# Kernel optimization log

Hardware: AMD Instinct MI355X
Metric: run time of the kernel (lower is better)

Reference implementation:

```python
import jax, jax.numpy as jnp
import numpy as np

# ---- architecture constants ----
SENSOR = 128          # u feature width
B_LAYERS = 5          # branch MLP: 4 tanh hidden + 1 linear out
B_UNITS = 1024
LORA = 64
TU = 128              # trunk hidden units
TL = 4                # trunk dense layers
TRUNK_DIMS = [1] + [TU] * (TL - 1) + [1]   # 1 -> 128 -> 128 -> 128 -> 1
NO_TRUNK_PARAMS = sum(d_out + d_in * d_out for d_in, d_out in zip(TRUNK_DIMS[:-1], TRUNK_DIMS[1:]))  # 33409
T0, TFINAL = 0.0, 1.0
BATCH = 2048


def setup_inputs() -> dict:
    key = jax.random.key(0)
    ks = jax.random.split(key, 16)
    def glorot(k, shape):
        fan_in, fan_out = shape[0], shape[1]
        s = jnp.sqrt(2.0 / (fan_in + fan_out)).astype(jnp.float32)
        return jax.random.normal(k, shape, dtype=jnp.float32) * s
    inp = {
        "t": jax.random.uniform(ks[0], (BATCH, 1), dtype=jnp.float32),
        "u": jax.random.normal(ks[1], (BATCH, SENSOR), dtype=jnp.float32),
        # branch MLP: Dense(1024)+tanh x4, then Dense(1024)
        "bw0": glorot(ks[2], (SENSOR, B_UNITS)), "bb0": jnp.zeros((B_UNITS,), jnp.float32),
        "bw1": glorot(ks[3], (B_UNITS, B_UNITS)), "bb1": jnp.zeros((B_UNITS,), jnp.float32),
        "bw2": glorot(ks[4], (B_UNITS, B_UNITS)), "bb2": jnp.zeros((B_UNITS,), jnp.float32),
        "bw3": glorot(ks[5], (B_UNITS, B_UNITS)), "bb3": jnp.zeros((B_UNITS,), jnp.float32),
        "bw4": glorot(ks[6], (B_UNITS, B_UNITS)), "bb4": jnp.zeros((B_UNITS,), jnp.float32),
        # LoRA factors generating trunk params
        "W1": glorot(ks[7], (B_UNITS, LORA)),
        "W2": glorot(ks[8], (LORA, NO_TRUNK_PARAMS)),
    }
    return inp


def _slice_trunk(p):
    """Split per-sample flat trunk params [B,P] into (kernel,bias) per layer.
    Flax tree_flatten order per Dense: bias then kernel."""
    layers = []
    k = 0
    for d_in, d_out in zip(TRUNK_DIMS[:-1], TRUNK_DIMS[1:]):
        b = p[:, k:k + d_out]; k += d_out
        W = p[:, k:k + d_in * d_out].reshape(-1, d_in, d_out); k += d_in * d_out
        layers.append((W, b))
    return layers


def reference(t, u, bw0, bb0, bw1, bb1, bw2, bb2, bw3, bb3, bw4, bb4, W1, W2):
    q0 = u[:, :1]                                     # [B,1]
    # branch MLP (hypernetwork body)
    net = u
    for W, b in ((bw0, bb0), (bw1, bb1), (bw2, bb2), (bw3, bb3)):
        net = jnp.tanh(net @ W + b)
    net = net @ bw4 + bb4                             # [B, units]
    # LoRA-generated per-sample trunk params
    params = net @ (W1 @ W2)                          # [B, NO_TRUNK_PARAMS]
    # batched per-sample trunk MLP on t[i] (vectorized form of the Python loop)
    x = t                                             # [B,1]
    trunk_layers = _slice_trunk(params)
    for i, (W, b) in enumerate(trunk_layers):
        x = jnp.einsum('bi,bio->bo', x, W) + b
        if i < TL - 1:
            x = jnp.tanh(x)
    q = x                                             # [B,1]
    # hard constraint: u0 + (t-t0)/(tfinal-t0)*nn
    out = q0 + (t - T0) / (TFINAL - T0) * q           # [B,1]
    return out.reshape(-1)
```

## Files before the change

kernel.cpp:

```cpp
#include <hip/hip_runtime.h>
#include <hip/hip_bf16.h>
#include <stdint.h>

typedef unsigned short u16;
typedef unsigned int   u32;
typedef short s16x8 __attribute__((ext_vector_type(8)));
typedef float f32x4 __attribute__((ext_vector_type(4)));

#define LDP 33409

__device__ __forceinline__ u16 f2bf(float f) {
    union { float f; u32 u; } v; v.f = f;
    u32 r = v.u + 0x7fffu + ((v.u >> 16) & 1u);
    return (u16)(r >> 16);
}
__device__ __forceinline__ float bf2f(u16 h) {
    union { u32 u; float f; } v; v.u = ((u32)h) << 16;
    return v.f;
}
__device__ __forceinline__ float fast_tanh(float x) {
    float e = __expf(2.0f * x);
    return 1.0f - 2.0f / (e + 1.0f);
}
__device__ __forceinline__ f32x4 MFMA(s16x8 a, s16x8 b, f32x4 c) {
    return __builtin_amdgcn_mfma_f32_16x16x32_bf16(a, b, c, 0, 0, 0);
}
__device__ __forceinline__ void gload_lds16(const void* g, void* l) {
    __builtin_amdgcn_global_load_lds(
        (const __attribute__((address_space(1))) u32*)(uintptr_t)g,
        (__attribute__((address_space(3))) u32*)(uintptr_t)l, 16, 0, 0);
}

__global__ __launch_bounds__(256, 2)
void gemm_l0(const float* __restrict__ u, const float* __restrict__ bw0,
             const float* __restrict__ bias, u16* __restrict__ Cout,
             const float* __restrict__ bw1, u16* __restrict__ bw1t)
{
    __shared__ __align__(16) char lds[24576];
    const int bid = blockIdx.x, tid = threadIdx.x;

    if (bid < 256) {
        u16 (*As)[128 * 32] = (u16(*)[128 * 32])lds;
        u16 (*Bs)[64 * 32]  = (u16(*)[64 * 32])(lds + 16384);
        const int lane = tid & 63, wid = tid >> 6;
        const int wr = wid >> 1, wc = wid & 1;
        const int bn = (bid & 15) * 64, bm = (bid >> 4) * 128;
        f32x4 acc[4][2] = {};

        auto STAGE = [&](int buf, int t) {
            const int k0 = t << 5;
            #pragma unroll
            for (int r = 0; r < 2; ++r) {
                int idx = r * 256 + tid;
                int row = idx >> 2, ck = idx & 3;
                const float* src = u + (size_t)(bm + row) * 128 + k0 + ck * 8;
                float4 x = *(const float4*)src;
                float4 y = *(const float4*)(src + 4);
                u16 o8[8] = {f2bf(x.x), f2bf(x.y), f2bf(x.z), f2bf(x.w),
                             f2bf(y.x), f2bf(y.y), f2bf(y.z), f2bf(y.w)};
                *(s16x8*)&As[buf][row * 32 + ((ck ^ (row & 3)) << 3)] = *(s16x8*)o8;
            }
            {
                int kk = tid >> 3, cg = tid & 7;
                const float* src = bw0 + (size_t)(k0 + kk) * 1024 + bn + cg * 8;
                float4 x = *(const float4*)src;
                float4 y = *(const float4*)(src + 4);
                float v[8] = {x.x, x.y, x.z, x.w, y.x, y.y, y.z, y.w};
                const int c = kk >> 3, e = kk & 7;
                #pragma unroll
                for (int j = 0; j < 8; ++j) {
                    int col = cg * 8 + j;
                    Bs[buf][col * 32 + ((c ^ (col & 3)) << 3) + e] = f2bf(v[j]);
                }
            }
        };
        auto COMPUTE = [&](int buf) {
            s16x8 av[4], bv[2];
            #pragma unroll
            for (int mi = 0; mi < 4; ++mi) {
                int row = wr * 64 + mi * 16 + (lane & 15);
                int s = (lane >> 4) ^ (row & 3);
                av[mi] = *(const s16x8*)&As[buf][row * 32 + s * 8];
            }
            #pragma unroll
            for (int ni = 0; ni < 2; ++ni) {
                int col = wc * 32 + ni * 16 + (lane & 15);
                int s = (lane >> 4) ^ (col & 3);
                bv[ni] = *(const s16x8*)&Bs[buf][col * 32 + s * 8];
            }
            #pragma unroll
            for (int mi = 0; mi < 4; ++mi)
            #pragma unroll
            for (int ni = 0; ni < 2; ++ni)
                acc[mi][ni] = MFMA(av[mi], bv[ni], acc[mi][ni]);
        };

        STAGE(0, 0);
        __syncthreads();
        #pragma unroll
        for (int t = 0; t < 4; ++t) {
            if (t + 1 < 4) STAGE((t + 1) & 1, t + 1);
            COMPUTE(t & 1);
            __syncthreads();
        }
        #pragma unroll
        for (int mi = 0; mi < 4; ++mi)
        #pragma unroll
        for (int ni = 0; ni < 2; ++ni) {
            const int col = bn + wc * 32 + ni * 16 + (lane & 15);
            const float bv = bias[col];
            #pragma unroll
            for (int jj = 0; jj < 4; ++jj) {
                const int row = bm + wr * 64 + mi * 16 + (lane >> 4) * 4 + jj;
                Cout[(size_t)row * 1024 + col] = f2bf(fast_tanh(acc[mi][ni][jj] + bv));
            }
        }
    } else {
        float (*tile)[65] = (float(*)[65])lds;
        const int idx = bid - 256;
        const int rb = (idx >> 4) * 64, cb = (idx & 15) * 64;
        for (int i = tid; i < 64 * 64; i += 256) {
            int r = i >> 6, c = i & 63;
            tile[r][c] = bw1[(size_t)(rb + r) * 1024 + cb + c];
        }
        __syncthreads();
        for (int i = tid; i < 64 * 64; i += 256) {
            int c = i >> 6, r = i & 63;
            bw1t[(size_t)(cb + c) * 1024 + rb + r] = f2bf(tile[r][c]);
        }
    }
}

__global__ __launch_bounds__(256, 2)
void gemm_fused(const u16* __restrict__ A, int lda,
                const u16* __restrict__ Bt, int ldb,
                const float* __restrict__ bias,
                u16* __restrict__ Cout, int ldc, int K, int mode,
                const float* __restrict__ xsrc, u16* __restrict__ xdst,
                const float* __restrict__ bw4, const float* __restrict__ bb4,
                const float* __restrict__ W1, u16* __restrict__ BWt,
                float* __restrict__ bz,
                const float* __restrict__ W2, u16* __restrict__ Btb)
{
    __shared__ __align__(16) char lds[24576];
    const int bid = blockIdx.x, tid = threadIdx.x;

    if (bid < 256) {
        u16 (*As)[128 * 32] = (u16(*)[128 * 32])lds;
        u16 (*Bs)[64 * 32]  = (u16(*)[64 * 32])(lds + 16384);
        const int lane = tid & 63, wid = tid >> 6;
        const int wr = wid >> 1, wc = wid & 1;
        const int bn = (bid & 15) * 64, bm = (bid >> 4) * 128;
        const int NT = K >> 5;
        const int arow = tid >> 2, ck = tid & 3;
        const u16* aSrc = A + (size_t)(bm + arow) * lda + (ck ^ (arow & 3)) * 8;
        const u16* bSrc = Bt + (size_t)(bn + arow) * ldb + (ck ^ (arow & 3)) * 8;
        const size_t aHalf = (size_t)64 * lda;
        f32x4 acc[4][2] = {};

        auto STAGE = [&](int buf, int t) {
            const int k0 = t << 5;
            gload_lds16(aSrc + k0,         (char*)As[buf] + wid * 1024);
            gload_lds16(aSrc + aHalf + k0, (char*)As[buf] + 4096 + wid * 1024);
            gload_lds16(bSrc + k0,         (char*)Bs[buf] + wid * 1024);
        };
        auto COMPUTE = [&](int buf) {
            s16x8 av[4], bv[2];
            #pragma unroll
            for (int mi = 0; mi < 4; ++mi) {
                int row = wr * 64 + mi * 16 + (lane & 15);
                int s = (lane >> 4) ^ (row & 3);
                av[mi] = *(const s16x8*)&As[buf][row * 32 + s * 8];
            }
            #pragma unroll
            for (int ni = 0; ni < 2; ++ni) {
                int col = wc * 32 + ni * 16 + (lane & 15);
                int s = (lane >> 4) ^ (col & 3);
                bv[ni] = *(const s16x8*)&Bs[buf][col * 32 + s * 8];
            }
            #pragma unroll
            for (int mi = 0; mi < 4; ++mi)
            #pragma unroll
            for (int ni = 0; ni < 2; ++ni)
                acc[mi][ni] = MFMA(av[mi], bv[ni], acc[mi][ni]);
        };

        STAGE(0, 0);
        __syncthreads();
        for (int t = 0; t < NT; ++t) {
            if (t + 1 < NT) STAGE((t + 1) & 1, t + 1);
            COMPUTE(t & 1);
            __syncthreads();
        }
        #pragma unroll
        for (int mi = 0; mi < 4; ++mi)
        #pragma unroll
        for (int ni = 0; ni < 2; ++ni) {
            const int col = bn + wc * 32 + ni * 16 + (lane & 15);
            const float bv = bias[col];
            #pragma unroll
            for (int jj = 0; jj < 4; ++jj) {
                const int row = bm + wr * 64 + mi * 16 + (lane >> 4) * 4 + jj;
                Cout[(size_t)row * ldc + col] = f2bf(fast_tanh(acc[mi][ni][jj] + bv));
            }
        }
    } else if (mode <= 2 && bid < 512) {
        float (*tile)[65] = (float(*)[65])lds;
        const int idx = bid - 256;
        const int rb = (idx >> 4) * 64, cb = (idx & 15) * 64;
        for (int i = tid; i < 64 * 64; i += 256) {
            int r = i >> 6, c = i & 63;
            tile[r][c] = xsrc[(size_t)(rb + r) * 1024 + cb + c];
        }
        __syncthreads();
        for (int i = tid; i < 64 * 64; i += 256) {
            int c = i >> 6, r = i & 63;
            xdst[(size_t)(cb + c) * 1024 + rb + r] = f2bf(tile[r][c]);
        }
    } else if (mode == 2) {
        const int lb = bid - 512;
        const int n = tid & 63, jc = tid >> 6;
        if (lb == 512) {
            float (*sh1)[64] = (float(*)[64])lds;
            float a = 0.f;
            for (int j = jc * 256; j < jc * 256 + 256; ++j)
                a = fmaf(bb4[j], W1[j * 64 + n], a);
            sh1[jc][n] = a;
            __syncthreads();
            if (tid < 64)
                bz[tid] = sh1[0][tid] + sh1[1][tid] + sh1[2][tid] + sh1[3][tid];
            return;
        }
        float (*sh)[2][64] = (float(*)[2][64])lds;
        const int k0 = lb * 2;
        float a0 = 0.f, a1 = 0.f;
        for (int j = jc * 256; j < jc * 256 + 256; ++j) {
            float w = W1[j * 64 + n];
            a0 = fmaf(bw4[(size_t)k0 * 1024 + j], w, a0);
            a1 = fmaf(bw4[(size_t)(k0 + 1) * 1024 + j], w, a1);
        }
        sh[jc][0][n] = a0; sh[jc][1][n] = a1;
        __syncthreads();
        if (tid < 128) {
            int kk = tid >> 6, nn = tid & 63;
            float s = sh[0][kk][nn] + sh[1][kk][nn] + sh[2][kk][nn] + sh[3][kk][nn];
            BWt[(size_t)nn * 1024 + k0 + kk] = f2bf(s);
        }
    } else {
        float (*tile)[130] = (float(*)[130])lds;
        const int idx = bid - 256;
        const int layer = idx / 258, pbi = idx % 258;
        u16* Btd = Btb + (size_t)layer * 128 * 8256;
        const int colbase = layer ? 16896 : 384, biasbase = layer ? 16768 : 256;
        const int pb = pbi * 32;
        for (int i = tid; i < 32 * 128; i += 256) {
            int p = pb + (i >> 7), n = i & 127;
            float v = (p < 8192)
                ? W2[(size_t)(p & 63) * LDP + colbase + (size_t)(p >> 6) * 128 + n]
                : W2[(size_t)(p - 8192) * LDP + biasbase + n];
            tile[i >> 7][n] = v;
        }
        __syncthreads();
        for (int i = tid; i < 32 * 128; i += 256) {
            int n = i >> 5, dp = i & 31;
            Btd[(size_t)n * 8256 + pb + dp] = f2bf(tile[dp][n]);
        }
    }
}

__global__ __launch_bounds__(256, 2)
void zgemm(const u16* __restrict__ A, const u16* __restrict__ Bt,
           float* __restrict__ zc)
{
    __shared__ __align__(16) u16 As[2][64 * 32];
    __shared__ __align__(16) u16 Bs[2][64 * 32];
    const int tid = threadIdx.x, lane = tid & 63, wid = tid >> 6;
    const int wr = wid >> 1, wc = wid & 1;
    const int bm = blockIdx.y * 64, kz = blockIdx.z;
    const int t0 = kz * 4, nt = 4;
    const int arow = tid >> 2, ck = tid & 3;
    const u16* aSrc = A + (size_t)(bm + arow) * 1024 + (ck ^ (arow & 3)) * 8;
    const u16* bSrc = Bt + (size_t)arow * 1024 + (ck ^ (arow & 3)) * 8;
    f32x4 acc[2][2] = {};

    auto STAGE = [&](int buf, int t) {
        const int k0 = t << 5;
        gload_lds16(aSrc + k0, (char*)As[buf] + wid * 1024);
        gload_lds16(bSrc + k0, (char*)Bs[buf] + wid * 1024);
    };
    auto COMPUTE = [&](int buf) {
        s16x8 a[2];
        #pragma unroll
        for (int mi = 0; mi < 2; ++mi) {
            int row = wr * 32 + mi * 16 + (lane & 15);
            int s = (lane >> 4) ^ (row & 3);
            a[mi] = *(const s16x8*)&As[buf][row * 32 + s * 8];
        }
        #pragma unroll
        for (int ni = 0; ni < 2; ++ni) {
            int n = wc * 32 + ni * 16 + (lane & 15);
            int s = (lane >> 4) ^ (n & 3);
            s16x8 b = *(const s16x8*)&Bs[buf][n * 32 + s * 8];
            #pragma unroll
            for (int mi = 0; mi < 2; ++mi)
                acc[mi][ni] = MFMA(a[mi], b, acc[mi][ni]);
        }
    };

    STAGE(0, t0);
    __syncthreads();
    for (int t = 0; t < nt; ++t) {
        if (t + 1 < nt) STAGE((t + 1) & 1, t0 + t + 1);
        COMPUTE(t & 1);
        __syncthreads();
    }
    #pragma unroll
    for (int mi = 0; mi < 2; ++mi)
    #pragma unroll
    for (int ni = 0; ni < 2; ++ni) {
        const int col = wc * 32 + ni * 16 + (lane & 15);
        #pragma unroll
        for (int jj = 0; jj < 4; ++jj) {
            const int row = bm + wr * 32 + mi * 16 + (lane >> 4) * 4 + jj;
            zc[((size_t)kz * 2048 + row) * 64 + col] = acc[mi][ni][jj];
        }
    }
}

__global__ __launch_bounds__(256)
void z_l1_h1(const float* __restrict__ zc, const float* __restrict__ bz,
             const float* __restrict__ W2, const float* __restrict__ t,
             u16* __restrict__ z, u16* __restrict__ h1)
{
    __shared__ float zsh[16][64];
    const int rb = blockIdx.x * 16;
    #pragma unroll
    for (int ii = 0; ii < 4; ++ii) {
        int e = ii * 256 + threadIdx.x;
        int r = e >> 6, k = e & 63;
        size_t off = (size_t)(rb + r) * 64 + k;
        float s = bz[k];
        #pragma unroll
        for (int sk = 0; sk < 8; ++sk) s += zc[(size_t)sk * 2048 * 64 + off];
        zsh[r][k] = s;
        z[off] = f2bf(s);
    }
    __syncthreads();
    const int o = threadIdx.x & 127;
    const int rh = (threadIdx.x >> 7) * 8;
    float acc_a[8] = {}, acc_b[8] = {};
    for (int k = 0; k < 64; ++k) {
        float wa = W2[(size_t)k * LDP + o];
        float wb = W2[(size_t)k * LDP + 128 + o];
        #pragma unroll
        for (int r = 0; r < 8; ++r) {
            float zv = zsh[rh + r][k];
            acc_a[r] = fmaf(zv, wa, acc_a[r]);
            acc_b[r] = fmaf(zv, wb, acc_b[r]);
        }
    }
    #pragma unroll
    for (int r = 0; r < 8; ++r) {
        int b = rb + rh + r;
        h1[b * 128 + o] = f2bf(fast_tanh(t[b] * acc_b[r] + acc_a[r]));
    }
}

__global__ __launch_bounds__(512, 2)
void trunk128(const u16* __restrict__ h, const u16* __restrict__ z,
              const u16* __restrict__ Bt, float* __restrict__ Cp)
{
    constexpr int NT = 258, SKT = 16;
    __shared__ __align__(16) u16 As[2][128 * 32];
    __shared__ __align__(16) u16 Bs[2][128 * 32];
    const int tid = threadIdx.x, lane = tid & 63, wid = tid >> 6;
    const int wr = wid >> 1, wc = wid & 1;
    const int bm = blockIdx.y * 128, kz = blockIdx.x;
    const int t0 = (NT * kz) / SKT, t1 = (NT * (kz + 1)) / SKT;
    const int arow = tid >> 2, ck = tid & 3;
    const int b = bm + arow;
    const s16x8 zlo = *(const s16x8*)&z[b * 64 + ck * 8];
    const s16x8 zhi = *(const s16x8*)&z[b * 64 + 32 + ck * 8];
    const int slot = (ck ^ (arow & 3)) * 8;
    f32x4 acc[2][4] = {};

    auto STAGE = [&](int buf, int t) {
        const int p0 = t << 5;
        gload_lds16(Bt + (size_t)arow * 8256 + p0 + (ck ^ (arow & 3)) * 8,
                    (char*)Bs[buf] + wid * 1024);
        const s16x8 zv = (p0 & 32) ? zhi : zlo;
        u16 o8[8];
        if (p0 < 8192) {
            const float hf = bf2f(h[b * 128 + (p0 >> 6)]);
            #pragma unroll
            for (int j = 0; j < 8; ++j) o8[j] = f2bf(hf * bf2f((u16)zv[j]));
        } else {
            #pragma unroll
            for (int j = 0; j < 8; ++j) o8[j] = (u16)zv[j];
        }
        *(s16x8*)&As[buf][arow * 32 + slot] = *(s16x8*)o8;
    };
    auto COMPUTE = [&](int buf) {
        s16x8 av[2], bb[4];
        #pragma unroll
        for (int mi = 0; mi < 2; ++mi) {
            int row = wr * 32 + mi * 16 + (lane & 15);
            int s = (lane >> 4) ^ (row & 3);
            av[mi] = *(const s16x8*)&As[buf][row * 32 + s * 8];
        }
        #pragma unroll
        for (int ni = 0; ni < 4; ++ni) {
            int n = wc * 64 + ni * 16 + (lane & 15);
            int s = (lane >> 4) ^ (n & 3);
            bb[ni] = *(const s16x8*)&Bs[buf][n * 32 + s * 8];
        }
        #pragma unroll
        for (int mi = 0; mi < 2; ++mi)
        #pragma unroll
        for (int ni = 0; ni < 4; ++ni)
            acc[mi][ni] = MFMA(av[mi], bb[ni], acc[mi][ni]);
    };

    STAGE(0, t0);
    __syncthreads();
    const int nt = t1 - t0;
    for (int t = 0; t < nt; ++t) {
        if (t + 1 < nt) STAGE((t + 1) & 1, t0 + t + 1);
        COMPUTE(t & 1);
        __syncthreads();
    }

    #pragma unroll
    for (int mi = 0; mi < 2; ++mi)
    #pragma unroll
    for (int ni = 0; ni < 4; ++ni) {
        const int col = wc * 64 + ni * 16 + (lane & 15);
        #pragma unroll
        for (int jj = 0; jj < 4; ++jj) {
            const int row = bm + wr * 32 + mi * 16 + (lane >> 4) * 4 + jj;
            Cp[((size_t)kz * 2048 + row) * 128 + col] = acc[mi][ni][jj];
        }
    }
}

__global__ __launch_bounds__(256)
void reduce_tanh(const float* __restrict__ Cp, u16* __restrict__ hout) {
    const int i4 = (blockIdx.x * 256 + threadIdx.x) * 4;
    const size_t S = (size_t)2048 * 128;
    float4 s = make_float4(0.f, 0.f, 0.f, 0.f);
    #pragma unroll
    for (int k = 0; k < 16; ++k) {
        float4 v = *(const float4*)&Cp[(size_t)k * S + i4];
        s.x += v.x; s.y += v.y; s.z += v.z; s.w += v.w;
    }
    uint2 o;
    o.x = (u32)f2bf(fast_tanh(s.x)) | ((u32)f2bf(fast_tanh(s.y)) << 16);
    o.y = (u32)f2bf(fast_tanh(s.z)) | ((u32)f2bf(fast_tanh(s.w)) << 16);
    *(uint2*)&hout[i4] = o;
}

__global__ __launch_bounds__(256)
void reduce_out(const float* __restrict__ Cp, const u16* __restrict__ z,
                const float* __restrict__ W2, const float* __restrict__ t,
                const float* __restrict__ u, float* __restrict__ out)
{
    __shared__ float sh[4][128];
    const int wv = threadIdx.x >> 6, l = threadIdx.x & 63;
    const int b = blockIdx.x * 4 + wv;
    const size_t S = (size_t)2048 * 128;
    #pragma unroll
    for (int e = l; e < 128; e += 64) {
        float s = 0.f;
        #pragma unroll
        for (int k = 0; k < 16; ++k) s += Cp[k * S + (size_t)b * 128 + e];
        sh[wv][e] = fast_tanh(s);
    }
    __syncthreads();
    const float* wrow = &W2[(size_t)l * LDP + 33280];
    float acc = wrow[0];
    #pragma unroll 8
    for (int i = 0; i < 128; ++i) acc = fmaf(sh[wv][i], wrow[1 + i], acc);
    float p = bf2f(z[b * 64 + l]) * acc;
    #pragma unroll
    for (int off = 32; off > 0; off >>= 1) p += __shfl_down(p, off);
    if (l == 0) out[b] = u[b * 128] + t[b] * p;
}

extern "C" void kernel_launch(void* const* d_in, const int* in_sizes, int n_in,
                              void* d_out, int out_size, void* d_ws, size_t ws_size,
                              hipStream_t stream)
{
    const float* t   = (const float*)d_in[0];
    const float* u   = (const float*)d_in[1];
    const float* bw0 = (const float*)d_in[2];
    const float* bb0 = (const float*)d_in[3];
    const float* bw1 = (const float*)d_in[4];
    const float* bb1 = (const float*)d_in[5];
    const float* bw2 = (const float*)d_in[6];
    const float* bb2 = (const float*)d_in[7];
    const float* bw3 = (const float*)d_in[8];
    const float* bb3 = (const float*)d_in[9];
    const float* bw4 = (const float*)d_in[10];
    const float* bb4 = (const float*)d_in[11];
    const float* W1  = (const float*)d_in[12];
    const float* W2  = (const float*)d_in[13];
    float* out = (float*)d_out;

    char* base = (char*)d_ws;
    u16*   bw1t = (u16*)(base);
    u16*   bw2t = (u16*)(base + 2097152);
    u16*   bw3t = (u16*)(base + 4194304);
    u16*   actA = (u16*)(base + 6291456);
    u16*   actB = (u16*)(base + 10485760);
    u16*   BWt  = (u16*)(base + 15499264);
    float* bz   = (float*)(base + 15630336);
    u16*   z    = (u16*)(base + 16777216);
    u16*   h1   = (u16*)(base + 17039360);
    u16*   h2   = (u16*)(base + 17563648);
    u16*   Bt   = (u16*)(base + 18087936);
    float* zc = (float*)(base);
    float* Cp = (float*)(base);

    dim3 blk(256);
    gemm_l0<<<512, blk, 0, stream>>>(u, bw0, bb0, actA, bw1, bw1t);
    gemm_fused<<<512, blk, 0, stream>>>(
        actA, 1024, bw1t, 1024, bb1, actB, 1024, 1024, 1,
        bw2, bw2t, bw4, bb4, W1, BWt, bz, W2, Bt);
    gemm_fused<<<1025, blk, 0, stream>>>(
        actB, 1024, bw2t, 1024, bb2, actA, 1024, 1024, 2,
        bw3, bw3t, bw4, bb4, W1, BWt, bz, W2, Bt);
    gemm_fused<<<772, blk, 0, stream>>>(
        actA, 1024, bw3t, 1024, bb3, actB, 1024, 1024, 3,
        nullptr, nullptr, bw4, bb4, W1, BWt, bz, W2, Bt);
    zgemm<<<dim3(1, 32, 8), blk, 0, stream>>>(actB, BWt, zc);
    z_l1_h1<<<128, blk, 0, stream>>>(zc, bz, W2, t, z, h1);
    trunk128<<<dim3(16, 16), dim3(512), 0, stream>>>(h1, z, Bt, Cp);
    reduce_tanh<<<256, blk, 0, stream>>>(Cp, h2);
    trunk128<<<dim3(16, 16), dim3(512), 0, stream>>>(h2, z, Bt + (size_t)128 * 8256, Cp);
    reduce_out<<<512, blk, 0, stream>>>(Cp, z, W2, t, u, out);
}
```

Before: 139.4 us.

## Move W2 trunk-weight prep to first kernel and fuse z GEMM into z_h1

The W2-to-bf16 transposition blocks move from the layer-3 launch into the first launch, so they overlap with layer-0 work. Layer 3 now runs in a dedicated 64x64-tile gemm_plain kernel with 512 blocks. The split-K zgemm and its partial-sum reduction are folded into z_h1, which computes the 16x64 z tile directly with MFMA before the h1 step. This removes one launch and the fp32 partial-sum round trip, at the cost of a long serial K loop per z_h1 block and smaller tiles for layer 3.

```diff
diff --git a/kernel.cpp b/kernel.cpp
--- a/kernel.cpp
+++ b/kernel.cpp
@@ -34,7 +34,8 @@
 __global__ __launch_bounds__(256, 2)
 void gemm_l0(const float* __restrict__ u, const float* __restrict__ bw0,
              const float* __restrict__ bias, u16* __restrict__ Cout,
-             const float* __restrict__ bw1, u16* __restrict__ bw1t)
+             const float* __restrict__ bw1, u16* __restrict__ bw1t,
+             const float* __restrict__ W2, u16* __restrict__ Btb)
 {
     __shared__ __align__(16) char lds[24576];
     const int bid = blockIdx.x, tid = threadIdx.x;
@@ -115,7 +116,7 @@
                 Cout[(size_t)row * 1024 + col] = f2bf(fast_tanh(acc[mi][ni][jj] + bv));
             }
         }
-    } else {
+    } else if (bid < 512) {
         float (*tile)[65] = (float(*)[65])lds;
         const int idx = bid - 256;
         const int rb = (idx >> 4) * 64, cb = (idx & 15) * 64;
@@ -127,6 +128,25 @@
         for (int i = tid; i < 64 * 64; i += 256) {
             int c = i >> 6, r = i & 63;
             bw1t[(size_t)(cb + c) * 1024 + rb + r] = f2bf(tile[r][c]);
+        }
+    } else {
+        float (*tile)[130] = (float(*)[130])lds;
+        const int idx = bid - 512;
+        const int layer = idx / 258, pbi = idx % 258;
+        u16* Btd = Btb + (size_t)layer * 128 * 8256;
+        const int colbase = layer ? 16896 : 384, biasbase = layer ? 16768 : 256;
+        const int pb = pbi * 32;
+        for (int i = tid; i < 32 * 128; i += 256) {
+            int p = pb + (i >> 7), n = i & 127;
+            float v = (p < 8192)
+                ? W2[(size_t)(p & 63) * LDP + colbase + (size_t)(p >> 6) * 128 + n]
+                : W2[(size_t)(p - 8192) * LDP + biasbase + n];
+            tile[i >> 7][n] = v;
+        }
+        __syncthreads();
+        for (int i = tid; i < 32 * 128; i += 256) {
+            int n = i >> 5, dp = i & 31;
+            Btd[(size_t)n * 8256 + pb + dp] = f2bf(tile[dp][n]);
         }
     }
 }
@@ -139,8 +159,7 @@
                 const float* __restrict__ xsrc, u16* __restrict__ xdst,
                 const float* __restrict__ bw4, const float* __restrict__ bb4,
                 const float* __restrict__ W1, u16* __restrict__ BWt,
-                float* __restrict__ bz,
-                const float* __restrict__ W2, u16* __restrict__ Btb)
+                float* __restrict__ bz)
 {
     __shared__ __align__(16) char lds[24576];
     const int bid = blockIdx.x, tid = threadIdx.x;
@@ -246,41 +265,21 @@
             float s = sh[0][kk][nn] + sh[1][kk][nn] + sh[2][kk][nn] + sh[3][kk][nn];
             BWt[(size_t)nn * 1024 + k0 + kk] = f2bf(s);
         }
-    } else {
-        float (*tile)[130] = (float(*)[130])lds;
-        const int idx = bid - 256;
-        const int layer = idx / 258, pbi = idx % 258;
-        u16* Btd = Btb + (size_t)layer * 128 * 8256;
-        const int colbase = layer ? 16896 : 384, biasbase = layer ? 16768 : 256;
-        const int pb = pbi * 32;
-        for (int i = tid; i < 32 * 128; i += 256) {
-            int p = pb + (i >> 7), n = i & 127;
-            float v = (p < 8192)
-                ? W2[(size_t)(p & 63) * LDP + colbase + (size_t)(p >> 6) * 128 + n]
-                : W2[(size_t)(p - 8192) * LDP + biasbase + n];
-            tile[i >> 7][n] = v;
-        }
-        __syncthreads();
-        for (int i = tid; i < 32 * 128; i += 256) {
-            int n = i >> 5, dp = i & 31;
-            Btd[(size_t)n * 8256 + pb + dp] = f2bf(tile[dp][n]);
-        }
     }
 }
 
 __global__ __launch_bounds__(256, 2)
-void zgemm(const u16* __restrict__ A, const u16* __restrict__ Bt,
-           float* __restrict__ zc)
+void gemm_plain(const u16* __restrict__ A, const u16* __restrict__ Bt,
+                const float* __restrict__ bias, u16* __restrict__ Cout)
 {
     __shared__ __align__(16) u16 As[2][64 * 32];
     __shared__ __align__(16) u16 Bs[2][64 * 32];
     const int tid = threadIdx.x, lane = tid & 63, wid = tid >> 6;
     const int wr = wid >> 1, wc = wid & 1;
-    const int bm = blockIdx.y * 64, kz = blockIdx.z;
-    const int t0 = kz * 4, nt = 4;
+    const int bn = blockIdx.x * 64, bm = blockIdx.y * 64;
     const int arow = tid >> 2, ck = tid & 3;
     const u16* aSrc = A + (size_t)(bm + arow) * 1024 + (ck ^ (arow & 3)) * 8;
-    const u16* bSrc = Bt + (size_t)arow * 1024 + (ck ^ (arow & 3)) * 8;
+    const u16* bSrc = Bt + (size_t)(bn + arow) * 1024 + (ck ^ (arow & 3)) * 8;
     f32x4 acc[2][2] = {};
 
     auto STAGE = [&](int buf, int t) {
@@ -289,7 +288,7 @@
         gload_lds16(bSrc + k0, (char*)Bs[buf] + wid * 1024);
     };
     auto COMPUTE = [&](int buf) {
-        s16x8 a[2];
+        s16x8 a[2], b[2];
         #pragma unroll
         for (int mi = 0; mi < 2; ++mi) {
             int row = wr * 32 + mi * 16 + (lane & 15);
@@ -300,17 +299,19 @@
         for (int ni = 0; ni < 2; ++ni) {
             int n = wc * 32 + ni * 16 + (lane & 15);
             int s = (lane >> 4) ^ (n & 3);
-            s16x8 b = *(const s16x8*)&Bs[buf][n * 32 + s * 8];
-            #pragma unroll
-            for (int mi = 0; mi < 2; ++mi)
-                acc[mi][ni] = MFMA(a[mi], b, acc[mi][ni]);
-        }
+            b[ni] = *(const s16x8*)&Bs[buf][n * 32 + s * 8];
+        }
+        #pragma unroll
+        for (int mi = 0; mi < 2; ++mi)
+        #pragma unroll
+        for (int ni = 0; ni < 2; ++ni)
+            acc[mi][ni] = MFMA(a[mi], b[ni], acc[mi][ni]);
     };
 
-    STAGE(0, t0);
+    STAGE(0, 0);
     __syncthreads();
-    for (int t = 0; t < nt; ++t) {
-        if (t + 1 < nt) STAGE((t + 1) & 1, t0 + t + 1);
+    for (int t = 0; t < 32; ++t) {
+        if (t + 1 < 32) STAGE((t + 1) & 1, t + 1);
         COMPUTE(t & 1);
         __syncthreads();
     }
@@ -318,36 +319,69 @@
     for (int mi = 0; mi < 2; ++mi)
     #pragma unroll
     for (int ni = 0; ni < 2; ++ni) {
-        const int col = wc * 32 + ni * 16 + (lane & 15);
+        const int col = bn + wc * 32 + ni * 16 + (lane & 15);
+        const float bv = bias[col];
         #pragma unroll
         for (int jj = 0; jj < 4; ++jj) {
             const int row = bm + wr * 32 + mi * 16 + (lane >> 4) * 4 + jj;
-            zc[((size_t)kz * 2048 + row) * 64 + col] = acc[mi][ni][jj];
+            Cout[(size_t)row * 1024 + col] = f2bf(fast_tanh(acc[mi][ni][jj] + bv));
         }
     }
 }
 
 __global__ __launch_bounds__(256)
-void z_l1_h1(const float* __restrict__ zc, const float* __restrict__ bz,
-             const float* __restrict__ W2, const float* __restrict__ t,
-             u16* __restrict__ z, u16* __restrict__ h1)
-{
+void z_h1(const u16* __restrict__ A, const u16* __restrict__ Bt,
+          const float* __restrict__ bz, const float* __restrict__ W2,
+          const float* __restrict__ t, u16* __restrict__ z,
+          u16* __restrict__ h1)
+{
+    __shared__ __align__(16) u16 As[2][16 * 32];
+    __shared__ __align__(16) u16 Bs[2][64 * 32];
     __shared__ float zsh[16][64];
+    const int tid = threadIdx.x, lane = tid & 63, wid = tid >> 6;
     const int rb = blockIdx.x * 16;
-    #pragma unroll
-    for (int ii = 0; ii < 4; ++ii) {
-        int e = ii * 256 + threadIdx.x;
-        int r = e >> 6, k = e & 63;
-        size_t off = (size_t)(rb + r) * 64 + k;
-        float s = bz[k];
-        #pragma unroll
-        for (int sk = 0; sk < 8; ++sk) s += zc[(size_t)sk * 2048 * 64 + off];
-        zsh[r][k] = s;
-        z[off] = f2bf(s);
-    }
+    const int brow = tid >> 2, bck = tid & 3;
+    const u16* bSrc = Bt + (size_t)brow * 1024 + (bck ^ (brow & 3)) * 8;
+    const int aRow = lane >> 2, ack = lane & 3;
+    const u16* aSrc = A + (size_t)(rb + aRow) * 1024 + (ack ^ (aRow & 3)) * 8;
+    f32x4 acc = {};
+
+    auto STAGE = [&](int buf, int tt) {
+        const int k0 = tt << 5;
+        if (wid == 0) gload_lds16(aSrc + k0, (char*)As[buf] + lane * 16);
+        gload_lds16(bSrc + k0, (char*)Bs[buf] + wid * 1024);
+    };
+    auto COMPUTE = [&](int buf) {
+        const int row = lane & 15;
+        const int sa = (lane >> 4) ^ (row & 3);
+        s16x8 av = *(const s16x8*)&As[buf][row * 32 + sa * 8];
+        const int col = wid * 16 + (lane & 15);
+        const int sb = (lane >> 4) ^ (col & 3);
+        s16x8 bv = *(const s16x8*)&Bs[buf][col * 32 + sb * 8];
+        acc = MFMA(av, bv, acc);
+    };
+
+    STAGE(0, 0);
     __syncthreads();
-    const int o = threadIdx.x & 127;
-    const int rh = (threadIdx.x >> 7) * 8;
+    for (int tt = 0; tt < 32; ++tt) {
+        if (tt + 1 < 32) STAGE((tt + 1) & 1, tt + 1);
+        COMPUTE(tt & 1);
+        __syncthreads();
+    }
+    {
+        const int col = wid * 16 + (lane & 15);
+        const float bzc = bz[col];
+        #pragma unroll
+        for (int j = 0; j < 4; ++j) {
+            const int row = (lane >> 4) * 4 + j;
+            float v = acc[j] + bzc;
+            zsh[row][col] = v;
+            z[(size_t)(rb + row) * 64 + col] = f2bf(v);
+        }
+    }
+    __syncthreads();
+    const int o = tid & 127;
+    const int rh = (tid >> 7) * 8;
     float acc_a[8] = {}, acc_b[8] = {};
     for (int k = 0; k < 64; ++k) {
         float wa = W2[(size_t)k * LDP + o];
@@ -518,22 +552,18 @@
     u16*   h1   = (u16*)(base + 17039360);
     u16*   h2   = (u16*)(base + 17563648);
     u16*   Bt   = (u16*)(base + 18087936);
-    float* zc = (float*)(base);
-    float* Cp = (float*)(base);
+    float* Cp   = (float*)(base);
 
     dim3 blk(256);
-    gemm_l0<<<512, blk, 0, stream>>>(u, bw0, bb0, actA, bw1, bw1t);
+    gemm_l0<<<1028, blk, 0, stream>>>(u, bw0, bb0, actA, bw1, bw1t, W2, Bt);
     gemm_fused<<<512, blk, 0, stream>>>(
         actA, 1024, bw1t, 1024, bb1, actB, 1024, 1024, 1,
-        bw2, bw2t, bw4, bb4, W1, BWt, bz, W2, Bt);
+        bw2, bw2t, bw4, bb4, W1, BWt, bz);
     gemm_fused<<<1025, blk, 0, stream>>>(
         actB, 1024, bw2t, 1024, bb2, actA, 1024, 1024, 2,
-        bw3, bw3t, bw4, bb4, W1, BWt, bz, W2, Bt);
-    gemm_fused<<<772, blk, 0, stream>>>(
-        actA, 1024, bw3t, 1024, bb3, actB, 1024, 1024, 3,
-        nullptr, nullptr, bw4, bb4, W1, BWt, bz, W2, Bt);
-    zgemm<<<dim3(1, 32, 8), blk, 0, stream>>>(actB, BWt, zc);
-    z_l1_h1<<<128, blk, 0, stream>>>(zc, bz, W2, t, z, h1);
+        bw3, bw3t, bw4, bb4, W1, BWt, bz);
+    gemm_plain<<<dim3(16, 32), blk, 0, stream>>>(actA, bw3t, bb3, actB);
+    z_h1<<<128, blk, 0, stream>>>(actB, BWt, bz, W2, t, z, h1);
     trunk128<<<dim3(16, 16), dim3(512), 0, stream>>>(h1, z, Bt, Cp);
     reduce_tanh<<<256, blk, 0, stream>>>(Cp, h2);
     trunk128<<<dim3(16, 16), dim3(512), 0, stream>>>(h2, z, Bt + (size_t)128 * 8256, Cp);
```

Measured after the change: 137.7 us. About the same (-1.2%).
